# Optimization experiments

Hardware: AMD Instinct MI355X
Metric: run time of the kernel (lower is better)

## Reference

```python
import jax, jax.numpy as jnp
import numpy as np

IN_FEATURES = 4096
OUT_FEATURES = 14336
BATCH = 2
SEQ = 2048
INT4_ZERO = 8  # stored uint-style int4 values in [0,16); signed value = q - 8


def setup_inputs() -> dict:
    key = jax.random.key(0)
    k_x, k_w, k_s, k_b = jax.random.split(key, 4)
    x = jax.random.normal(k_x, (BATCH, SEQ, IN_FEATURES), dtype=jnp.float32)
    weight_q = jax.random.randint(k_w, (OUT_FEATURES, IN_FEATURES), 0, 16, dtype=jnp.int32)
    weight_scale = jax.random.uniform(k_s, (OUT_FEATURES, 1), dtype=jnp.float32)
    bias = jax.random.normal(k_b, (OUT_FEATURES,), dtype=jnp.float32)
    return {"x": x, "weight_q": weight_q, "weight_scale": weight_scale, "bias": bias}


def reference(x, weight_q, weight_scale, bias):
    orig_shape = x.shape
    x2d = x.reshape(-1, orig_shape[-1])  # [T, in]
    # fused int4 dequant + matmul + bias: w = (q - zero) * per-row scale
    w = (weight_q.astype(x.dtype) - INT4_ZERO) * weight_scale  # [out, in]
    y2d = jnp.einsum('ti,oi->to', x2d, w) + bias  # [T, out]
    return y2d.reshape(*orig_shape[:-1], w.shape[0])
```

## Files before the change

kernel.cpp:

```cpp
#include <hip/hip_runtime.h>
#include <hip/hip_bf16.h>


#define AS1 __attribute__((address_space(1)))
#define AS3 __attribute__((address_space(3)))

typedef __attribute__((ext_vector_type(8))) short short8;
typedef __attribute__((ext_vector_type(4))) float f32x4;

static constexpr int IN_F   = 4096;
static constexpr int OUT_F  = 14336;
static constexpr int TOKENS = 2 * 2048;


__device__ __forceinline__ unsigned short bf16_rne(float f) {
    unsigned int u = __float_as_uint(f);
    u += 0x7fffu + ((u >> 16) & 1u);
    return (unsigned short)(u >> 16);
}

__global__ void convert_x_kernel(const float4* __restrict__ x,
                                 ushort4* __restrict__ xb) {
    size_t i = (size_t)blockIdx.x * blockDim.x + threadIdx.x;
    float4 v = x[i];
    ushort4 r;
    r.x = bf16_rne(v.x); r.y = bf16_rne(v.y);
    r.z = bf16_rne(v.z); r.w = bf16_rne(v.w);
    xb[i] = r;
}

__global__ void convert_w_kernel(const int4* __restrict__ q,
                                 ushort4* __restrict__ wb) {
    size_t i = (size_t)blockIdx.x * blockDim.x + threadIdx.x;
    int4 v = q[i];
    ushort4 r;
    r.x = (unsigned short)(__float_as_uint((float)(v.x - 8)) >> 16);
    r.y = (unsigned short)(__float_as_uint((float)(v.y - 8)) >> 16);
    r.z = (unsigned short)(__float_as_uint((float)(v.z - 8)) >> 16);
    r.w = (unsigned short)(__float_as_uint((float)(v.w - 8)) >> 16);
    wb[i] = r;
}


__global__ __launch_bounds__(256)
void gemm_bt_kernel(const unsigned short* __restrict__ A,
                    const unsigned short* __restrict__ B,
                    const float* __restrict__ scale,
                    const float* __restrict__ bias,
                    float* __restrict__ C) {
    constexpr int K  = IN_F;
    constexpr int N  = OUT_F;
    constexpr int BM = 128, BN = 128, BK = 32;

    __shared__ __align__(16) unsigned short sA[BM * BK];
    __shared__ __align__(16) unsigned short sB[BN * BK];

    const int tid  = threadIdx.x;
    const int wave = tid >> 6;
    const int lane = tid & 63;
    const int l16  = lane & 15;
    const int lq   = lane >> 4;

    const int mBase = blockIdx.y * BM;
    const int nBase = blockIdx.x * BN;
    const int wm = (wave >> 1) * 64;
    const int wn = (wave & 1) * 64;

    const int sr = tid >> 2;
    const int sc = (tid & 3) * 8;

    const unsigned short* gA = A + (size_t)(mBase + sr) * K + sc;
    const unsigned short* gB = B + (size_t)(nBase + sr) * K + sc;
    unsigned short* lA = &sA[sr * BK + sc];
    unsigned short* lB = &sB[sr * BK + sc];

    f32x4 acc[4][4] = {};

    for (int k0 = 0; k0 < K; k0 += BK) {
        __builtin_amdgcn_global_load_lds((const AS1 void*)(gA + k0),
                                         (AS3 void*)lA, 16, 0, 0);
        __builtin_amdgcn_global_load_lds((const AS1 void*)(gA + (size_t)64 * K + k0),
                                         (AS3 void*)(lA + 64 * BK), 16, 0, 0);
        __builtin_amdgcn_global_load_lds((const AS1 void*)(gB + k0),
                                         (AS3 void*)lB, 16, 0, 0);
        __builtin_amdgcn_global_load_lds((const AS1 void*)(gB + (size_t)64 * K + k0),
                                         (AS3 void*)(lB + 64 * BK), 16, 0, 0);
        __syncthreads();

        short8 af[4], bfr[4];
#pragma unroll
        for (int i = 0; i < 4; ++i)
            af[i] = *(const short8*)&sA[(wm + i * 16 + l16) * BK + lq * 8];
#pragma unroll
        for (int j = 0; j < 4; ++j)
            bfr[j] = *(const short8*)&sB[(wn + j * 16 + l16) * BK + lq * 8];

#pragma unroll
        for (int i = 0; i < 4; ++i)
#pragma unroll
            for (int j = 0; j < 4; ++j)
                acc[i][j] = __builtin_amdgcn_mfma_f32_16x16x32_bf16(
                    af[i], bfr[j], acc[i][j], 0, 0, 0);
        __syncthreads();
    }

#pragma unroll
    for (int j = 0; j < 4; ++j) {
        const int n = nBase + wn + j * 16 + l16;
        const float s  = scale[n];
        const float bb = bias[n];
#pragma unroll
        for (int i = 0; i < 4; ++i) {
            const int m0 = mBase + wm + i * 16 + lq * 4;
#pragma unroll
            for (int r = 0; r < 4; ++r)
                C[(size_t)(m0 + r) * N + n] = acc[i][j][r] * s + bb;
        }
    }
}


extern "C" void kernel_launch(void* const* d_in, const int* in_sizes, int n_in,
                              void* d_out, int out_size, void* d_ws, size_t ws_size,
                              hipStream_t stream) {
    const float* x      = (const float*)d_in[0];
    const int*   wq     = (const int*)d_in[1];
    const float* wscale = (const float*)d_in[2];
    const float* wbias  = (const float*)d_in[3];
    float* out = (float*)d_out;

    unsigned short* wbf = (unsigned short*)d_ws;
    unsigned short* xbf = wbf + (size_t)OUT_F * IN_F;

    convert_w_kernel<<<57344, 256, 0, stream>>>((const int4*)wq, (ushort4*)wbf);
    convert_x_kernel<<<16384, 256, 0, stream>>>((const float4*)x, (ushort4*)xbf);

    dim3 grid(OUT_F / 128, TOKENS / 128);
    gemm_bt_kernel<<<grid, 256, 0, stream>>>(xbf, wbf, wscale, wbias, out);
}
```

Baseline: 942.0 us.

## Replace GEMM with 256x256 double-buffered LDS pipeline and fuse convert kernels

Merges the weight and activation conversion kernels into one launch. Replaces the 128x128 single-buffered GEMM with a 256x256-tile, 512-thread kernel that uses BK=64, double-buffered LDS staging via global_load_lds, XOR-swizzled LDS layout, fine-grained interleaving of loads with MFMA quads, s_setprio, and a block-index swizzle for L2 locality. It targets the memory-stall and barrier overhead of the old loop and raises data reuse per tile. The cost is higher register and LDS pressure plus complex hand-written wait counts that could be fragile.

```diff
diff --git a/kernel.cpp b/kernel.cpp
--- a/kernel.cpp
+++ b/kernel.cpp
@@ -1,5 +1,4 @@
 #include <hip/hip_runtime.h>
-#include <hip/hip_bf16.h>
 
 
 #define AS1 __attribute__((address_space(1)))
@@ -10,7 +9,7 @@
 
 static constexpr int IN_F   = 4096;
 static constexpr int OUT_F  = 14336;
-static constexpr int TOKENS = 2 * 2048;
+static constexpr int TOKENS = 4096;
 
 
 __device__ __forceinline__ unsigned short bf16_rne(float f) {
@@ -19,102 +18,172 @@
     return (unsigned short)(u >> 16);
 }
 
-__global__ void convert_x_kernel(const float4* __restrict__ x,
-                                 ushort4* __restrict__ xb) {
+__global__ void convert_kernel(const int4* __restrict__ q, ushort4* __restrict__ wb,
+                               const float4* __restrict__ x, ushort4* __restrict__ xb) {
+    constexpr size_t NW = (size_t)OUT_F * IN_F / 4;
     size_t i = (size_t)blockIdx.x * blockDim.x + threadIdx.x;
-    float4 v = x[i];
-    ushort4 r;
-    r.x = bf16_rne(v.x); r.y = bf16_rne(v.y);
-    r.z = bf16_rne(v.z); r.w = bf16_rne(v.w);
-    xb[i] = r;
-}
-
-__global__ void convert_w_kernel(const int4* __restrict__ q,
-                                 ushort4* __restrict__ wb) {
-    size_t i = (size_t)blockIdx.x * blockDim.x + threadIdx.x;
-    int4 v = q[i];
-    ushort4 r;
-    r.x = (unsigned short)(__float_as_uint((float)(v.x - 8)) >> 16);
-    r.y = (unsigned short)(__float_as_uint((float)(v.y - 8)) >> 16);
-    r.z = (unsigned short)(__float_as_uint((float)(v.z - 8)) >> 16);
-    r.w = (unsigned short)(__float_as_uint((float)(v.w - 8)) >> 16);
-    wb[i] = r;
-}
-
-
-__global__ __launch_bounds__(256)
-void gemm_bt_kernel(const unsigned short* __restrict__ A,
+    if (i < NW) {
+        int4 v = q[i];
+        ushort4 r;
+        r.x = (unsigned short)(__float_as_uint((float)(v.x - 8)) >> 16);
+        r.y = (unsigned short)(__float_as_uint((float)(v.y - 8)) >> 16);
+        r.z = (unsigned short)(__float_as_uint((float)(v.z - 8)) >> 16);
+        r.w = (unsigned short)(__float_as_uint((float)(v.w - 8)) >> 16);
+        wb[i] = r;
+    } else {
+        size_t j = i - NW;
+        float4 v = x[j];
+        ushort4 r;
+        r.x = bf16_rne(v.x); r.y = bf16_rne(v.y);
+        r.z = bf16_rne(v.z); r.w = bf16_rne(v.w);
+        xb[j] = r;
+    }
+}
+
+
+#define STAGE(T_, Q_, MATP_)                                                               \
+    do {                                                                                   \
+        const unsigned short* g_ = ((Q_) < 2 ? gA : gB) + ((Q_) & 1) * (size_t)(128 * K)   \
+                                   + (size_t)(T_) * BK;                                    \
+        unsigned short* l_ = (MATP_) + ((Q_) & 1) * HS + tid * 8;                          \
+        __builtin_amdgcn_global_load_lds((const AS1 void*)g_, (AS3 void*)l_, 16, 0, 0);    \
+        __builtin_amdgcn_global_load_lds((const AS1 void*)(g_ + (size_t)64 * K),           \
+                                         (AS3 void*)(l_ + 4096), 16, 0, 0);                \
+    } while (0)
+
+#define BAR()                                                                              \
+    do {                                                                                   \
+        asm volatile("" ::: "memory");                                                     \
+        __builtin_amdgcn_s_barrier();                                                      \
+        asm volatile("" ::: "memory");                                                     \
+    } while (0)
+
+#define MFMA_QUAD(M0_, N0_)                                                                \
+    __builtin_amdgcn_s_setprio(1);                                                         \
+    _Pragma("unroll") for (int s_ = 0; s_ < 2; ++s_)                                       \
+        _Pragma("unroll") for (int m_ = 0; m_ < 4; ++m_)                                   \
+            _Pragma("unroll") for (int n_ = 0; n_ < 2; ++n_)                               \
+                acc[(M0_) + m_][(N0_) + n_] = __builtin_amdgcn_mfma_f32_16x16x32_bf16(     \
+                    af[(M0_) + m_][s_], bf[(N0_) + n_][s_],                                \
+                    acc[(M0_) + m_][(N0_) + n_], 0, 0, 0);                                 \
+    __builtin_amdgcn_s_setprio(0);
+
+#define KTILE(T_, TA_, TB_, NXA_, NXB_)                                                    \
+    do {                                                                                   \
+             \
+        _Pragma("unroll") for (int m_ = 0; m_ < 4; ++m_) {                                 \
+            af[m_][0] = *(const short8*)((TA_) + aOff + m_ * 1024);                        \
+            af[m_][1] = *(const short8*)((TA_) + aOff + m_ * 1024 + 32);                   \
+        }                                                                                  \
+        _Pragma("unroll") for (int n_ = 0; n_ < 2; ++n_) {                                 \
+            bf[n_][0] = *(const short8*)((TB_) + bOff + n_ * 1024);                        \
+            bf[n_][1] = *(const short8*)((TB_) + bOff + n_ * 1024 + 32);                   \
+        }                                                                                  \
+        if ((T_) + 1 < NT) STAGE((T_) + 1, 2, NXB_);                                       \
+        BAR();                                                                             \
+        asm volatile("s_waitcnt lgkmcnt(0)" ::: "memory");                                 \
+        MFMA_QUAD(0, 0)                                                                    \
+        BAR();                                                                             \
+                            \
+        _Pragma("unroll") for (int m_ = 0; m_ < 4; ++m_) {                                 \
+            af[4 + m_][0] = *(const short8*)((TA_) + aOff + (4 + m_) * 1024);              \
+            af[4 + m_][1] = *(const short8*)((TA_) + aOff + (4 + m_) * 1024 + 32);         \
+        }                                                                                  \
+        _Pragma("unroll") for (int n_ = 0; n_ < 2; ++n_) {                                 \
+            bf[2 + n_][0] = *(const short8*)((TB_) + bOff + (2 + n_) * 1024);              \
+            bf[2 + n_][1] = *(const short8*)((TB_) + bOff + (2 + n_) * 1024 + 32);         \
+        }                                                                                  \
+        if ((T_) + 1 < NT) STAGE((T_) + 1, 3, NXB_);                                       \
+        BAR();                                                                             \
+        asm volatile("s_waitcnt lgkmcnt(0)" ::: "memory");                                 \
+        MFMA_QUAD(4, 0)                                                                    \
+        BAR();                                                                             \
+                                        \
+        if ((T_) + 2 < NT) STAGE((T_) + 2, 0, NXA_);                                       \
+        BAR();                                                                             \
+        MFMA_QUAD(0, 2)                                                                    \
+        BAR();                                                                             \
+                         \
+        if ((T_) + 2 < NT) STAGE((T_) + 2, 1, NXA_);                                       \
+        BAR();                                                                             \
+        MFMA_QUAD(4, 2)                                                                    \
+        if ((T_) + 2 < NT) {                                                               \
+            asm volatile("s_waitcnt vmcnt(4)" ::: "memory");                               \
+        } else {                                                                           \
+            asm volatile("s_waitcnt vmcnt(0)" ::: "memory");                               \
+        }                                                                                  \
+        BAR();                                                                             \
+    } while (0)
+
+__global__ __launch_bounds__(512, 2)
+void gemm256_kernel(const unsigned short* __restrict__ A,
                     const unsigned short* __restrict__ B,
                     const float* __restrict__ scale,
                     const float* __restrict__ bias,
                     float* __restrict__ C) {
     constexpr int K  = IN_F;
     constexpr int N  = OUT_F;
-    constexpr int BM = 128, BN = 128, BK = 32;
-
-    __shared__ __align__(16) unsigned short sA[BM * BK];
-    __shared__ __align__(16) unsigned short sB[BN * BK];
+    constexpr int BK = 64;
+    constexpr int NT = K / BK;
+    constexpr int TS = 256 * BK;
+    constexpr int HS = TS / 2;
+
+    __shared__ unsigned short sm[2][2][TS];
 
     const int tid  = threadIdx.x;
+    const int lane = tid & 63;
     const int wave = tid >> 6;
-    const int lane = tid & 63;
     const int l16  = lane & 15;
     const int lq   = lane >> 4;
-
-    const int mBase = blockIdx.y * BM;
-    const int nBase = blockIdx.x * BN;
-    const int wm = (wave >> 1) * 64;
-    const int wn = (wave & 1) * 64;
-
-    const int sr = tid >> 2;
-    const int sc = (tid & 3) * 8;
-
-    const unsigned short* gA = A + (size_t)(mBase + sr) * K + sc;
-    const unsigned short* gB = B + (size_t)(nBase + sr) * K + sc;
-    unsigned short* lA = &sA[sr * BK + sc];
-    unsigned short* lB = &sB[sr * BK + sc];
-
-    f32x4 acc[4][4] = {};
-
-    for (int k0 = 0; k0 < K; k0 += BK) {
-        __builtin_amdgcn_global_load_lds((const AS1 void*)(gA + k0),
-                                         (AS3 void*)lA, 16, 0, 0);
-        __builtin_amdgcn_global_load_lds((const AS1 void*)(gA + (size_t)64 * K + k0),
-                                         (AS3 void*)(lA + 64 * BK), 16, 0, 0);
-        __builtin_amdgcn_global_load_lds((const AS1 void*)(gB + k0),
-                                         (AS3 void*)lB, 16, 0, 0);
-        __builtin_amdgcn_global_load_lds((const AS1 void*)(gB + (size_t)64 * K + k0),
-                                         (AS3 void*)(lB + 64 * BK), 16, 0, 0);
-        __syncthreads();
-
-        short8 af[4], bfr[4];
+    const int wr   = wave >> 2;
+    const int wc   = wave & 3;
+
+    const int bid   = blockIdx.y * 56 + blockIdx.x;
+    const int swz   = (bid & 7) * 112 + (bid >> 3);
+    const int nBase = (swz % 56) * 256;
+    const int mBase = (swz / 56) * 256;
+
+    const int cs   = tid ^ (((tid >> 5) & 1) << 1);
+    const int srow = cs >> 3;
+    const int scol = (cs & 7) * 8;
+    const unsigned short* gA = A + (size_t)(mBase + srow) * K + scol;
+    const unsigned short* gB = B + (size_t)(nBase + srow) * K + scol;
+
+    const int klane = lq ^ ((l16 >> 1) & 2);
+    const int aOff  = (wr * 128 + l16) * 64 + klane * 8;
+    const int bOff  = (wc * 64  + l16) * 64 + klane * 8;
+
+    f32x4  acc[8][4] = {};
+    short8 af[8][2];
+    short8 bf[4][2];
+
+    unsigned short* smA0 = &sm[0][0][0];
+    unsigned short* smB0 = &sm[0][1][0];
+    unsigned short* smA1 = &sm[1][0][0];
+    unsigned short* smB1 = &sm[1][1][0];
+
+    STAGE(0, 0, smA0); STAGE(0, 1, smA0); STAGE(0, 2, smB0); STAGE(0, 3, smB0);
+    STAGE(1, 0, smA1); STAGE(1, 1, smA1);
+    asm volatile("s_waitcnt vmcnt(4)" ::: "memory");
+    BAR();
+
+    for (int t = 0; t < NT; t += 2) {
+        KTILE(t,     smA0, smB0, smA0, smB1);
+        KTILE(t + 1, smA1, smB1, smA1, smB0);
+    }
+
 #pragma unroll
-        for (int i = 0; i < 4; ++i)
-            af[i] = *(const short8*)&sA[(wm + i * 16 + l16) * BK + lq * 8];
+    for (int n = 0; n < 4; ++n) {
+        const int col  = nBase + wc * 64 + n * 16 + l16;
+        const float s  = scale[col];
+        const float bb = bias[col];
 #pragma unroll
-        for (int j = 0; j < 4; ++j)
-            bfr[j] = *(const short8*)&sB[(wn + j * 16 + l16) * BK + lq * 8];
-
-#pragma unroll
-        for (int i = 0; i < 4; ++i)
-#pragma unroll
-            for (int j = 0; j < 4; ++j)
-                acc[i][j] = __builtin_amdgcn_mfma_f32_16x16x32_bf16(
-                    af[i], bfr[j], acc[i][j], 0, 0, 0);
-        __syncthreads();
-    }
-
-#pragma unroll
-    for (int j = 0; j < 4; ++j) {
-        const int n = nBase + wn + j * 16 + l16;
-        const float s  = scale[n];
-        const float bb = bias[n];
-#pragma unroll
-        for (int i = 0; i < 4; ++i) {
-            const int m0 = mBase + wm + i * 16 + lq * 4;
+        for (int m = 0; m < 8; ++m) {
+            const int row0 = mBase + wr * 128 + m * 16 + lq * 4;
+            float* cp = C + (size_t)row0 * N + col;
 #pragma unroll
             for (int r = 0; r < 4; ++r)
-                C[(size_t)(m0 + r) * N + n] = acc[i][j][r] * s + bb;
+                cp[(size_t)r * N] = acc[m][n][r] * s + bb;
         }
     }
 }
@@ -132,9 +201,8 @@
     unsigned short* wbf = (unsigned short*)d_ws;
     unsigned short* xbf = wbf + (size_t)OUT_F * IN_F;
 
-    convert_w_kernel<<<57344, 256, 0, stream>>>((const int4*)wq, (ushort4*)wbf);
-    convert_x_kernel<<<16384, 256, 0, stream>>>((const float4*)x, (ushort4*)xbf);
-
-    dim3 grid(OUT_F / 128, TOKENS / 128);
-    gemm_bt_kernel<<<grid, 256, 0, stream>>>(xbf, wbf, wscale, wbias, out);
-}
+    convert_kernel<<<73728, 256, 0, stream>>>((const int4*)wq, (ushort4*)wbf,
+                                              (const float4*)x, (ushort4*)xbf);
+
+    gemm256_kernel<<<dim3(56, 16), 512, 0, stream>>>(xbf, wbf, wscale, wbias, out);
+}
```

After: 905.4 us. 3.9% less time.
